# Performance work log

Hardware: AMD Instinct MI355X
Metric: run time of the kernel (lower is better)

## Reference

```python
import jax, jax.numpy as jnp
import numpy as np

NUM_SLOTS = 8
SLOT_DIM = 3
WRITE_RATE = 0.1


def _amu(x, memory, Wk, bk, Ww, bw, Wg, bg, Wo, bo):
    """Associative Memory Unit.
    x: [B, T, Din], memory: [B, N, D] -> (outputs [B, T, Dout], memory [B, N, D]).
    Per step: softmax key-addressing read, gated erase/add write at WRITE_RATE,
    output = Linear(concat(x_t, read)).
    """
    xt = jnp.swapaxes(x, 0, 1)  # [T, B, Din]

    def step(mem, x_t):
        k = x_t @ Wk + bk                                   # [B, D]
        scores = jnp.einsum('bnd,bd->bn', mem, k)           # [B, N]
        w = jax.nn.softmax(scores, axis=-1)                 # addressing weights
        read = jnp.einsum('bn,bnd->bd', w, mem)             # [B, D]
        v = x_t @ Ww + bw                                   # write vector [B, D]
        e = jax.nn.sigmoid(x_t @ Wg + bg)                   # erase gate [B, D]
        we = w[:, :, None] * e[:, None, :]                  # [B, N, D]
        mem = mem * (1.0 - WRITE_RATE * we) + WRITE_RATE * w[:, :, None] * v[:, None, :]
        out = jnp.concatenate([x_t, read], axis=-1) @ Wo + bo
        return mem, out

    mem, outs = jax.lax.scan(step, memory, xt)
    return jnp.swapaxes(outs, 0, 1), mem


def setup_inputs() -> dict:
    key = jax.random.key(0)
    ks = jax.random.split(key, 12)
    B, T, D_in, D_hid, D_out = 64, 512, 128, 512, 128
    s = 0.05
    return {
        'inp': jax.random.normal(ks[0], (B, T, D_in), jnp.float32),
        'W1k': jax.random.normal(ks[1], (D_in, SLOT_DIM), jnp.float32) * s,
        'b1k': jnp.zeros((SLOT_DIM,), jnp.float32),
        'W1w': jax.random.normal(ks[2], (D_in, SLOT_DIM), jnp.float32) * s,
        'b1w': jnp.zeros((SLOT_DIM,), jnp.float32),
        'W1g': jax.random.normal(ks[3], (D_in, SLOT_DIM), jnp.float32) * s,
        'b1g': jnp.zeros((SLOT_DIM,), jnp.float32),
        'W1o': jax.random.normal(ks[4], (D_in + SLOT_DIM, D_hid), jnp.float32) * s,
        'b1o': jnp.zeros((D_hid,), jnp.float32),
        'W2k': jax.random.normal(ks[5], (D_hid, SLOT_DIM), jnp.float32) * s,
        'b2k': jnp.zeros((SLOT_DIM,), jnp.float32),
        'W2w': jax.random.normal(ks[6], (D_hid, SLOT_DIM), jnp.float32) * s,
        'b2w': jnp.zeros((SLOT_DIM,), jnp.float32),
        'W2g': jax.random.normal(ks[7], (D_hid, SLOT_DIM), jnp.float32) * s,
        'b2g': jnp.zeros((SLOT_DIM,), jnp.float32),
        'W2o': jax.random.normal(ks[8], (D_hid + SLOT_DIM, D_out), jnp.float32) * s,
        'b2o': jnp.zeros((D_out,), jnp.float32),
    }


def reference(inp, W1k, b1k, W1w, b1w, W1g, b1g, W1o, b1o,
              W2k, b2k, W2w, b2w, W2g, b2g, W2o, b2o):
    B = inp.shape[0]
    mem0 = jnp.zeros((B, NUM_SLOTS, SLOT_DIM), inp.dtype)
    o1, mem = _amu(inp, mem0, W1k, b1k, W1w, b1w, W1g, b1g, W1o, b1o)
    o1 = jax.nn.sigmoid(o1)  # self.layers = Sequential(Sigmoid())
    o2, mem = _amu(o1, mem, W2k, b2k, W2w, b2w, W2g, b2g, W2o, b2o)
    out = jax.nn.sigmoid(o2[:, -1, :])  # last timestep, then sigmoid
    return out
```

## Files before the change

### kernel.cpp

```cpp
#include <hip/hip_runtime.h>
#include <hip/hip_bf16.h>

#define B_ 64
#define T_ 512
#define LOG2E 1.4426950408889634f
#define PHASE_STEPS 16
#define NPHASE (T_/PHASE_STEPS)

typedef __attribute__((ext_vector_type(8))) short short8;
typedef __attribute__((ext_vector_type(4))) float f32x4;

__device__ __forceinline__ float fast_exp2(float x){ return __builtin_amdgcn_exp2f(x); }
__device__ __forceinline__ float fast_rcp(float x){ return __builtin_amdgcn_rcpf(x); }
__device__ __forceinline__ float sigmoidf_(float x){ return fast_rcp(1.0f + fast_exp2(-x*LOG2E)); }
__device__ __forceinline__ unsigned short f2bf(float f){
  union{float f; unsigned u;} v; v.f = f;
  unsigned r = v.u + 0x7fffu + ((v.u>>16)&1u);
  return (unsigned short)(r>>16);
}

template<int CTRL>
__device__ __forceinline__ float dpp_xadd(float x){
  int y = __builtin_amdgcn_update_dpp(0, __float_as_int(x), CTRL, 0xf, 0xf, true);
  return x + __int_as_float(y);
}
__device__ __forceinline__ float dpp_sum8(float x){
  x = dpp_xadd<0xB1>(x);
  x = dpp_xadd<0x4E>(x);
  x = dpp_xadd<0x141>(x);
  return x;
}

__global__ __launch_bounds__(256) void k_prep(const float* __restrict__ W1o,
    const float* __restrict__ W2k, const float* __restrict__ W2w, const float* __restrict__ W2g,
    unsigned short* __restrict__ W1oTb, unsigned short* __restrict__ W2cTb)
{
  int idx = blockIdx.x*256 + threadIdx.x;
  if (idx < 65536){
    int n = idx >> 7, k = idx & 127;
    W1oTb[idx] = f2bf(W1o[k*512 + n]);
  }
  if (idx < 8192){
    int j = idx >> 9, c = idx & 511;
    float v = 0.f;
    if (j < 3) v = W2k[c*3 + j];
    else if (j < 6) v = W2w[c*3 + j - 3];
    else if (j < 9) v = W2g[c*3 + j - 6];
    W2cTb[idx] = f2bf(v);
  }
}

__global__ __launch_bounds__(256) void k_proj1(const float* __restrict__ X,
    const float* __restrict__ Wk, const float* __restrict__ bk,
    const float* __restrict__ Ww, const float* __restrict__ bw,
    const float* __restrict__ Wg, const float* __restrict__ bg,
    float* __restrict__ P1)
{
  __shared__ __align__(16) float A[64*132];
  __shared__ float Wc[128*12];
  __shared__ float bb[9];
  int tid = threadIdx.x;
  long r0 = (long)blockIdx.x * 64;
  const float4* X4 = (const float4*)(X + r0*128);
  #pragma unroll
  for (int it=0; it<8; ++it){
    int f4 = tid + it*256;
    float4 v = X4[f4];
    int f = f4*4; int row = f>>7; int k = f&127;
    A[row*132+k]   = v.x; A[row*132+k+1] = v.y;
    A[row*132+k+2] = v.z; A[row*132+k+3] = v.w;
  }
  #pragma unroll
  for (int it=0; it<5; ++it){
    int w = tid + it*256;
    if (w < 1152){
      int k = w/9, j = w%9;
      float val;
      if (j<3) val = Wk[k*3+j]; else if (j<6) val = Ww[k*3+j-3]; else val = Wg[k*3+j-6];
      Wc[k*12+j] = val;
    }
  }
  if (tid < 9){
    float v; if (tid<3) v = bk[tid]; else if (tid<6) v = bw[tid-3]; else v = bg[tid-6];
    bb[tid] = v;
  }
  __syncthreads();
  for (int o = tid; o < 576; o += 256){
    int row = o/9, j = o%9;
    float acc = bb[j];
    #pragma unroll 8
    for (int k=0;k<128;++k) acc = fmaf(A[row*132+k], Wc[k*12+j], acc);
    if (j<3) acc *= LOG2E;
    else if (j<6) acc *= 0.1f;
    else acc = 0.1f * sigmoidf_(acc);
    long r = r0 + row;
    int b = (int)(r >> 9); int t = (int)(r & 511);
    int bh = b >> 5, bl = b & 31;
    P1[((long)bh*512 + t)*288 + j*32 + bl] = acc;
  }
}

template<int STORE_ALL>
__device__ __forceinline__ void scan8(const float* __restrict__ P,
                                      float* __restrict__ Rout, int bh)
{
  __shared__ __align__(16) float buf[2][PHASE_STEPS*288];
  int tid = threadIdx.x;
  int wv = tid >> 6, lane = tid & 63;
  const float* Pb = P + (long)bh*512*288;
  if (wv == 4){
    #pragma unroll 1
    for (int p = 0; p < NPHASE; ++p){
      const float4* src = (const float4*)(Pb + (long)p*PHASE_STEPS*288);
      float4* dst = (float4*)buf[p&1];
      float4 tmp[18];
      #pragma unroll
      for (int i=0;i<18;++i) tmp[i] = src[lane + i*64];
      #pragma unroll
      for (int i=0;i<18;++i) dst[lane + i*64] = tmp[i];
      __syncthreads();
    }
  } else {
    int g = lane >> 3, slot = lane & 7;
    int bl = wv*8 + g;
    int batch = bh*32 + bl;
    float m0=0.f, m1=0.f, m2=0.f;
    __syncthreads();
    #pragma unroll 1
    for (int p = 0; p < NPHASE; ++p){
      const float* bp = buf[p&1];
      float pp[3][9];
      #pragma unroll
      for (int j=0;j<9;++j){ pp[0][j] = bp[j*32+bl]; pp[1][j] = bp[288 + j*32+bl]; }
      #pragma unroll
      for (int s=0;s<PHASE_STEPS;++s){
        if (s+2 < PHASE_STEPS){
          #pragma unroll
          for (int j=0;j<9;++j) pp[(s+2)%3][j] = bp[(s+2)*288 + j*32 + bl];
        }
        const float* pv = pp[s%3];
        float sc = fmaf(m2, pv[2], fmaf(m1, pv[1], m0*pv[0]));
        float pe = fast_exp2(sc);
        float S = dpp_sum8(pe);
        float rinv = fast_rcp(S);
        float w = pe * rinv;
        if (STORE_ALL){
          float r0 = dpp_sum8(pe*m0);
          float r1 = dpp_sum8(pe*m1);
          float r2 = dpp_sum8(pe*m2);
          float rsel = (slot==0) ? r0 : ((slot==1) ? r1 : r2);
          rsel *= rinv;
          if (slot < 3) Rout[((p*PHASE_STEPS+s)*3 + slot)*64 + batch] = rsel;
        } else if (s == PHASE_STEPS-1){
          if (p == NPHASE-1){
            float r0 = dpp_sum8(pe*m0);
            float r1 = dpp_sum8(pe*m1);
            float r2 = dpp_sum8(pe*m2);
            float rsel = (slot==0) ? r0 : ((slot==1) ? r1 : r2);
            rsel *= rinv;
            if (slot < 3) Rout[slot*64 + batch] = rsel;
          }
        }
        float v0=pv[3], v1=pv[4], v2=pv[5], e0=pv[6], e1=pv[7], e2=pv[8];
        m0 = fmaf(w, fmaf(-e0, m0, v0), m0);
        m1 = fmaf(w, fmaf(-e1, m1, v1), m1);
        m2 = fmaf(w, fmaf(-e2, m2, v2), m2);
      }
      if (p < NPHASE-1) __syncthreads();
    }
  }
}

__global__ __launch_bounds__(320) void k_scan1(const float* __restrict__ P1,
                                               float* __restrict__ R1)
{
  scan8<1>(P1, R1, (int)blockIdx.x);
}

__global__ __launch_bounds__(256) void k_fused(const float* __restrict__ X,
    const float* __restrict__ W1o, const float* __restrict__ b1o,
    const float* __restrict__ R1,
    const unsigned short* __restrict__ W1oTb, const unsigned short* __restrict__ W2cTb,
    const float* __restrict__ b2k, const float* __restrict__ b2w, const float* __restrict__ b2g,
    float* __restrict__ P2, float* __restrict__ O1last)
{
  __shared__ __align__(16) float rdS[48];
  __shared__ __align__(16) unsigned short o1b[16*520];
  __shared__ __align__(16) float pSum[4*16*16];
  int tid = threadIdx.x;
  int w = tid >> 6, lane = tid & 63;
  int n16 = lane & 15, g4 = lane >> 4;
  long r0 = (long)blockIdx.x * 16;
  int b = (int)(r0 >> 9); int t0 = (int)(r0 & 511);

  if (tid < 48){
    int i = tid/3, d = tid%3;
    rdS[tid] = R1[((t0+i)*3+d)*64 + b];
  }

  short8 afr[4];
  const float* Xrow = X + (r0 + n16)*128;
  #pragma unroll
  for (int q=0;q<4;++q){
    f32x4 x0 = *(const f32x4*)(Xrow + q*32 + g4*8);
    f32x4 x1 = *(const f32x4*)(Xrow + q*32 + g4*8 + 4);
    short8 a;
    a[0]=(short)f2bf(x0[0]); a[1]=(short)f2bf(x0[1]);
    a[2]=(short)f2bf(x0[2]); a[3]=(short)f2bf(x0[3]);
    a[4]=(short)f2bf(x1[0]); a[5]=(short)f2bf(x1[1]);
    a[6]=(short)f2bf(x1[2]); a[7]=(short)f2bf(x1[3]);
    afr[q]=a;
  }
  __syncthreads();

  f32x4 ra = *(const f32x4*)(rdS + g4*12);
  f32x4 rb = *(const f32x4*)(rdS + g4*12 + 4);
  f32x4 rc = *(const f32x4*)(rdS + g4*12 + 8);
  float rd0[4] = { ra[0], ra[3], rb[2], rc[1] };
  float rd1[4] = { ra[1], rb[0], rb[3], rc[2] };
  float rd2[4] = { ra[2], rb[1], rc[0], rc[3] };

  #pragma unroll
  for (int tt=0; tt<8; ++tt){
    int gc = w*128 + tt*16 + n16;
    f32x4 acc = {0.f,0.f,0.f,0.f};
    #pragma unroll
    for (int q=0;q<4;++q){
      short8 bf = *(const short8*)(W1oTb + gc*128 + q*32 + g4*8);
      acc = __builtin_amdgcn_mfma_f32_16x16x32_bf16(afr[q], bf, acc, 0,0,0);
    }
    float bias = b1o[gc];
    float wr0 = W1o[128*512+gc], wr1 = W1o[129*512+gc], wr2 = W1o[130*512+gc];
    #pragma unroll
    for (int reg=0; reg<4; ++reg){
      int rowloc = g4*4 + reg;
      float z = acc[reg] + bias + rd0[reg]*wr0 + rd1[reg]*wr1 + rd2[reg]*wr2;
      float o1 = sigmoidf_(z);
      o1b[rowloc*520 + gc] = f2bf(o1);
      if (t0 == 496 && rowloc == 15) O1last[b*512 + gc] = o1;
    }
  }

  f32x4 accP = {0.f,0.f,0.f,0.f};
  #pragma unroll
  for (int q2=0; q2<4; ++q2){
    int kk = w*128 + q2*32;
    short8 a2 = *(const short8*)(o1b + n16*520 + kk + g4*8);
    short8 bb2 = *(const short8*)(W2cTb + n16*512 + kk + g4*8);
    accP = __builtin_amdgcn_mfma_f32_16x16x32_bf16(a2, bb2, accP, 0,0,0);
  }
  #pragma unroll
  for (int reg=0;reg<4;++reg){
    int rowloc = g4*4+reg;
    pSum[w*256 + rowloc*16 + n16] = accP[reg];
  }
  __syncthreads();
  if (tid < 144){
    int r = tid/9, j = tid%9;
    float s = pSum[r*16+j] + pSum[256+r*16+j] + pSum[512+r*16+j] + pSum[768+r*16+j];
    float outv;
    if (j<3){ s += b2k[j]; outv = s*LOG2E; }
    else if (j<6){ s += b2w[j-3]; outv = 0.1f*s; }
    else { s += b2g[j-6]; outv = 0.1f*sigmoidf_(s); }
    int t = t0 + r;
    int bh = b >> 5, bl = b & 31;
    P2[((long)bh*512 + t)*288 + j*32 + bl] = outv;
  }
}

__global__ __launch_bounds__(320) void k_scan2_opart(const float* __restrict__ P2,
    float* __restrict__ R2F,
    const float* __restrict__ O1last, const float* __restrict__ W2o,
    const float* __restrict__ b2o, float* __restrict__ Opart)
{
  if (blockIdx.x < 2){
    scan8<0>(P2, R2F, (int)blockIdx.x);
    return;
  }
  __shared__ __align__(16) float s2[512];
  int b = blockIdx.x - 2; int tid = threadIdx.x;
  if (tid < 128)
    ((float4*)s2)[tid] = ((const float4*)(O1last + b*512))[tid];
  __syncthreads();
  if (tid < 128){
    float acc = b2o[tid];
    #pragma unroll 8
    for (int n=0;n<512;++n) acc = fmaf(s2[n], W2o[n*128+tid], acc);
    Opart[b*128+tid] = acc;
  }
}

__global__ __launch_bounds__(256) void k_final(const float* __restrict__ Opart,
    const float* __restrict__ R2F, const float* __restrict__ W2o,
    float* __restrict__ out)
{
  int idx = blockIdx.x*256 + threadIdx.x;
  if (idx < 8192){
    int b = idx >> 7; int o = idx & 127;
    float r0 = R2F[b], r1 = R2F[64+b], r2 = R2F[128+b];
    float v = Opart[idx]
            + r0*W2o[512*128+o] + r1*W2o[513*128+o] + r2*W2o[514*128+o];
    out[idx] = sigmoidf_(v);
  }
}

extern "C" void kernel_launch(void* const* d_in, const int* in_sizes, int n_in,
                              void* d_out, int out_size, void* d_ws, size_t ws_size,
                              hipStream_t stream)
{
  const float* X  = (const float*)d_in[0];
  const float* W1k= (const float*)d_in[1]; const float* b1k=(const float*)d_in[2];
  const float* W1w= (const float*)d_in[3]; const float* b1w=(const float*)d_in[4];
  const float* W1g= (const float*)d_in[5]; const float* b1g=(const float*)d_in[6];
  const float* W1o= (const float*)d_in[7]; const float* b1o=(const float*)d_in[8];
  const float* W2k= (const float*)d_in[9]; const float* b2k=(const float*)d_in[10];
  const float* W2w= (const float*)d_in[11]; const float* b2w=(const float*)d_in[12];
  const float* W2g= (const float*)d_in[13]; const float* b2g=(const float*)d_in[14];
  const float* W2o= (const float*)d_in[15]; const float* b2o=(const float*)d_in[16];

  float* ws = (float*)d_ws;
  float* P1     = ws;
  float* R1     = P1 + 294912;
  float* P2     = R1 + 98304;
  float* O1last = P2 + 294912;
  float* R2F    = O1last + 32768;
  float* Opart  = R2F + 192;
  unsigned short* W1oTb = (unsigned short*)(Opart + 8192);
  unsigned short* W2cTb = W1oTb + 65536;
  float* out    = (float*)d_out;

  hipLaunchKernelGGL(k_prep, dim3(256), dim3(256), 0, stream,
                     W1o, W2k, W2w, W2g, W1oTb, W2cTb);
  hipLaunchKernelGGL(k_proj1, dim3(512), dim3(256), 0, stream,
                     X, W1k,b1k, W1w,b1w, W1g,b1g, P1);
  hipLaunchKernelGGL(k_scan1, dim3(2), dim3(320), 0, stream, P1, R1);
  hipLaunchKernelGGL(k_fused, dim3(2048), dim3(256), 0, stream,
                     X, W1o, b1o, R1, W1oTb, W2cTb, b2k, b2w, b2g, P2, O1last);
  hipLaunchKernelGGL(k_scan2_opart, dim3(66), dim3(320), 0, stream,
                     P2, R2F, O1last, W2o, b2o, Opart);
  hipLaunchKernelGGL(k_final, dim3(32), dim3(256), 0, stream,
                     Opart, R2F, W2o, out);
}
```

Measured before the change: 260.7 us.

## Fuse pipeline into persistent megakernel with flag-based producer-consumer overlap

Result: slower. 346.9 us (+33.1%).

```diff
diff --git a/kernel.cpp b/kernel.cpp
--- a/kernel.cpp
+++ b/kernel.cpp
@@ -31,86 +31,30 @@
   return x;
 }
 
-__global__ __launch_bounds__(256) void k_prep(const float* __restrict__ W1o,
-    const float* __restrict__ W2k, const float* __restrict__ W2w, const float* __restrict__ W2g,
-    unsigned short* __restrict__ W1oTb, unsigned short* __restrict__ W2cTb)
+__device__ __forceinline__ unsigned ld_acq(unsigned* p){
+  return __hip_atomic_load(p, __ATOMIC_ACQUIRE, __HIP_MEMORY_SCOPE_AGENT);
+}
+__device__ __forceinline__ void spin_ge(unsigned* p, unsigned tgt){
+  while (ld_acq(p) < tgt) __builtin_amdgcn_s_sleep(4);
+}
+__device__ __forceinline__ void flag_add(unsigned* p){
+  __threadfence();
+  __hip_atomic_fetch_add(p, 1u, __ATOMIC_RELEASE, __HIP_MEMORY_SCOPE_AGENT);
+}
+
+template<int STORE_ALL>
+__device__ __forceinline__ void scan_role(const float* __restrict__ P,
+    float* __restrict__ Rout, int bh,
+    unsigned* cnt_in, unsigned tgt, unsigned* cnt_out, char* smemc)
 {
-  int idx = blockIdx.x*256 + threadIdx.x;
-  if (idx < 65536){
-    int n = idx >> 7, k = idx & 127;
-    W1oTb[idx] = f2bf(W1o[k*512 + n]);
-  }
-  if (idx < 8192){
-    int j = idx >> 9, c = idx & 511;
-    float v = 0.f;
-    if (j < 3) v = W2k[c*3 + j];
-    else if (j < 6) v = W2w[c*3 + j - 3];
-    else if (j < 9) v = W2g[c*3 + j - 6];
-    W2cTb[idx] = f2bf(v);
-  }
-}
-
-__global__ __launch_bounds__(256) void k_proj1(const float* __restrict__ X,
-    const float* __restrict__ Wk, const float* __restrict__ bk,
-    const float* __restrict__ Ww, const float* __restrict__ bw,
-    const float* __restrict__ Wg, const float* __restrict__ bg,
-    float* __restrict__ P1)
-{
-  __shared__ __align__(16) float A[64*132];
-  __shared__ float Wc[128*12];
-  __shared__ float bb[9];
-  int tid = threadIdx.x;
-  long r0 = (long)blockIdx.x * 64;
-  const float4* X4 = (const float4*)(X + r0*128);
-  #pragma unroll
-  for (int it=0; it<8; ++it){
-    int f4 = tid + it*256;
-    float4 v = X4[f4];
-    int f = f4*4; int row = f>>7; int k = f&127;
-    A[row*132+k]   = v.x; A[row*132+k+1] = v.y;
-    A[row*132+k+2] = v.z; A[row*132+k+3] = v.w;
-  }
-  #pragma unroll
-  for (int it=0; it<5; ++it){
-    int w = tid + it*256;
-    if (w < 1152){
-      int k = w/9, j = w%9;
-      float val;
-      if (j<3) val = Wk[k*3+j]; else if (j<6) val = Ww[k*3+j-3]; else val = Wg[k*3+j-6];
-      Wc[k*12+j] = val;
-    }
-  }
-  if (tid < 9){
-    float v; if (tid<3) v = bk[tid]; else if (tid<6) v = bw[tid-3]; else v = bg[tid-6];
-    bb[tid] = v;
-  }
-  __syncthreads();
-  for (int o = tid; o < 576; o += 256){
-    int row = o/9, j = o%9;
-    float acc = bb[j];
-    #pragma unroll 8
-    for (int k=0;k<128;++k) acc = fmaf(A[row*132+k], Wc[k*12+j], acc);
-    if (j<3) acc *= LOG2E;
-    else if (j<6) acc *= 0.1f;
-    else acc = 0.1f * sigmoidf_(acc);
-    long r = r0 + row;
-    int b = (int)(r >> 9); int t = (int)(r & 511);
-    int bh = b >> 5, bl = b & 31;
-    P1[((long)bh*512 + t)*288 + j*32 + bl] = acc;
-  }
-}
-
-template<int STORE_ALL>
-__device__ __forceinline__ void scan8(const float* __restrict__ P,
-                                      float* __restrict__ Rout, int bh)
-{
-  __shared__ __align__(16) float buf[2][PHASE_STEPS*288];
+  float (*buf)[PHASE_STEPS*288] = (float (*)[PHASE_STEPS*288])smemc;
   int tid = threadIdx.x;
   int wv = tid >> 6, lane = tid & 63;
   const float* Pb = P + (long)bh*512*288;
   if (wv == 4){
     #pragma unroll 1
     for (int p = 0; p < NPHASE; ++p){
+      spin_ge(&cnt_in[p], tgt);
       const float4* src = (const float4*)(Pb + (long)p*PHASE_STEPS*288);
       float4* dst = (float4*)buf[p&1];
       float4 tmp[18];
@@ -120,6 +64,7 @@
       for (int i=0;i<18;++i) dst[lane + i*64] = tmp[i];
       __syncthreads();
     }
+    __syncthreads();
   } else {
     int g = lane >> 3, slot = lane & 7;
     int bl = wv*8 + g;
@@ -151,157 +96,223 @@
           float rsel = (slot==0) ? r0 : ((slot==1) ? r1 : r2);
           rsel *= rinv;
           if (slot < 3) Rout[((p*PHASE_STEPS+s)*3 + slot)*64 + batch] = rsel;
-        } else if (s == PHASE_STEPS-1){
-          if (p == NPHASE-1){
-            float r0 = dpp_sum8(pe*m0);
-            float r1 = dpp_sum8(pe*m1);
-            float r2 = dpp_sum8(pe*m2);
-            float rsel = (slot==0) ? r0 : ((slot==1) ? r1 : r2);
-            rsel *= rinv;
-            if (slot < 3) Rout[slot*64 + batch] = rsel;
-          }
+        } else if (s == PHASE_STEPS-1 && p == NPHASE-1){
+          float r0 = dpp_sum8(pe*m0);
+          float r1 = dpp_sum8(pe*m1);
+          float r2 = dpp_sum8(pe*m2);
+          float rsel = (slot==0) ? r0 : ((slot==1) ? r1 : r2);
+          rsel *= rinv;
+          if (slot < 3) Rout[slot*64 + batch] = rsel;
         }
         float v0=pv[3], v1=pv[4], v2=pv[5], e0=pv[6], e1=pv[7], e2=pv[8];
         m0 = fmaf(w, fmaf(-e0, m0, v0), m0);
         m1 = fmaf(w, fmaf(-e1, m1, v1), m1);
         m2 = fmaf(w, fmaf(-e2, m2, v2), m2);
       }
-      if (p < NPHASE-1) __syncthreads();
+      __syncthreads();
+      if (cnt_out && tid == 0) flag_add(&cnt_out[p]);
     }
   }
 }
 
-__global__ __launch_bounds__(320) void k_scan1(const float* __restrict__ P1,
-                                               float* __restrict__ R1)
+__global__ __launch_bounds__(320,1) void k_mega(
+    const float* __restrict__ X,
+    const float* __restrict__ W1k, const float* __restrict__ b1k,
+    const float* __restrict__ W1w, const float* __restrict__ b1w,
+    const float* __restrict__ W1g, const float* __restrict__ b1g,
+    const float* __restrict__ W1o, const float* __restrict__ b1o,
+    const float* __restrict__ W2k, const float* __restrict__ b2k,
+    const float* __restrict__ W2w, const float* __restrict__ b2w,
+    const float* __restrict__ W2g, const float* __restrict__ b2g,
+    float* __restrict__ P1, float* __restrict__ R1,
+    float* __restrict__ P2, float* __restrict__ O1last, float* __restrict__ R2F,
+    unsigned short* __restrict__ W1oTb, unsigned short* __restrict__ W2cTb,
+    unsigned* __restrict__ flags)
 {
-  scan8<1>(P1, R1, (int)blockIdx.x);
-}
-
-__global__ __launch_bounds__(256) void k_fused(const float* __restrict__ X,
-    const float* __restrict__ W1o, const float* __restrict__ b1o,
-    const float* __restrict__ R1,
-    const unsigned short* __restrict__ W1oTb, const unsigned short* __restrict__ W2cTb,
-    const float* __restrict__ b2k, const float* __restrict__ b2w, const float* __restrict__ b2g,
-    float* __restrict__ P2, float* __restrict__ O1last)
+  __shared__ __align__(16) char smem[40448];
+  unsigned* proj_cnt  = flags;
+  unsigned* r1_cnt    = flags + 32;
+  unsigned* fused_cnt = flags + 64;
+  unsigned* prep_cnt  = flags + 96;
+  int role = blockIdx.x;
+  int tid = threadIdx.x;
+
+  if (role < 2){ scan_role<1>(P1, R1, role, proj_cnt, 16, r1_cnt, smem); return; }
+  if (role < 4){ scan_role<0>(P2, R2F, role-2, fused_cnt, 64, nullptr, smem); return; }
+
+  int wid = role - 4;
+  int NW = (int)gridDim.x - 4;
+
+  {
+    int NT = NW*320;
+    int gthread = wid*320 + tid;
+    for (int x = gthread; x < 65536; x += NT){
+      int n = x >> 7, k = x & 127;
+      W1oTb[x] = f2bf(W1o[k*512 + n]);
+    }
+    for (int x = gthread; x < 8192; x += NT){
+      int j = x >> 9, cc = x & 511;
+      float v = 0.f;
+      if (j < 3) v = W2k[cc*3+j];
+      else if (j < 6) v = W2w[cc*3+j-3];
+      else if (j < 9) v = W2g[cc*3+j-6];
+      W2cTb[x] = f2bf(v);
+    }
+    __syncthreads();
+    if (tid == 0) flag_add(prep_cnt);
+  }
+
+  {
+    float* A  = (float*)smem;
+    float* Wc = (float*)(smem + 33792);
+    float* bb = (float*)(smem + 39936);
+    for (int w_=tid; w_<1152; w_+=320){
+      int k=w_/9, j=w_%9; float val;
+      if (j<3) val=W1k[k*3+j]; else if (j<6) val=W1w[k*3+j-3]; else val=W1g[k*3+j-6];
+      Wc[k*12+j]=val;
+    }
+    if (tid<9){ float v; if(tid<3)v=b1k[tid]; else if(tid<6)v=b1w[tid-3]; else v=b1g[tid-6]; bb[tid]=v; }
+    __syncthreads();
+    #pragma unroll 1
+    for (int i = wid; i < 512; i += NW){
+      int c = i >> 4, q = i & 15;
+      if (tid < 256){
+        #pragma unroll
+        for (int it=0; it<8; ++it){
+          int f4 = tid + it*256;
+          int blk = f4 >> 9, off = f4 & 511;
+          const float4* src = (const float4*)(X + ((long)(4*q+blk)*512 + 16*c)*128);
+          float4 v = src[off];
+          int f = off*4, trow = f>>7, k = f&127;
+          int row = blk*16 + trow;
+          A[row*132+k]=v.x; A[row*132+k+1]=v.y; A[row*132+k+2]=v.z; A[row*132+k+3]=v.w;
+        }
+      }
+      __syncthreads();
+      for (int o = tid; o < 576; o += 320){
+        int row=o/9, j=o%9;
+        float acc = bb[j];
+        #pragma unroll 8
+        for (int k=0;k<128;++k) acc = fmaf(A[row*132+k], Wc[k*12+j], acc);
+        if (j<3) acc *= LOG2E;
+        else if (j<6) acc *= 0.1f;
+        else acc = 0.1f*sigmoidf_(acc);
+        int b = 4*q + (row>>4), t = 16*c + (row&15);
+        P1[((long)(b>>5)*512 + t)*288 + j*32 + (b&31)] = acc;
+      }
+      __syncthreads();
+      if (tid == 0) flag_add(&proj_cnt[c]);
+    }
+  }
+
+  if (tid == 0) spin_ge(prep_cnt, (unsigned)NW);
+  __syncthreads();
+
+  {
+    float* pSum = (float*)smem;
+    float* rdS  = (float*)(smem + 4096);
+    unsigned short* o1b = (unsigned short*)(smem + 4352);
+    int w = tid >> 6, lane = tid & 63;
+    int n16 = lane & 15, g4 = lane >> 4;
+    #pragma unroll 1
+    for (int i = wid; i < 2048; i += NW){
+      int c = i >> 6, b = i & 63;
+      if (tid == 0) spin_ge(&r1_cnt[c], 2);
+      __syncthreads();
+      int t0 = c*16;
+      long r0 = (long)b*512 + t0;
+      if (tid < 48){
+        int ii = tid/3, d = tid%3;
+        rdS[tid] = R1[((t0+ii)*3+d)*64 + b];
+      }
+      short8 afr[4];
+      if (w < 4){
+        const float* Xrow = X + (r0 + n16)*128;
+        #pragma unroll
+        for (int q=0;q<4;++q){
+          f32x4 x0 = *(const f32x4*)(Xrow + q*32 + g4*8);
+          f32x4 x1 = *(const f32x4*)(Xrow + q*32 + g4*8 + 4);
+          short8 a;
+          a[0]=(short)f2bf(x0[0]); a[1]=(short)f2bf(x0[1]);
+          a[2]=(short)f2bf(x0[2]); a[3]=(short)f2bf(x0[3]);
+          a[4]=(short)f2bf(x1[0]); a[5]=(short)f2bf(x1[1]);
+          a[6]=(short)f2bf(x1[2]); a[7]=(short)f2bf(x1[3]);
+          afr[q]=a;
+        }
+      }
+      __syncthreads();
+      if (w < 4){
+        f32x4 ra = *(const f32x4*)(rdS + g4*12);
+        f32x4 rb = *(const f32x4*)(rdS + g4*12 + 4);
+        f32x4 rc = *(const f32x4*)(rdS + g4*12 + 8);
+        float rd0[4] = { ra[0], ra[3], rb[2], rc[1] };
+        float rd1[4] = { ra[1], rb[0], rb[3], rc[2] };
+        float rd2[4] = { ra[2], rb[1], rc[0], rc[3] };
+        #pragma unroll
+        for (int tt=0; tt<8; ++tt){
+          int gc = w*128 + tt*16 + n16;
+          f32x4 acc = {0.f,0.f,0.f,0.f};
+          #pragma unroll
+          for (int q=0;q<4;++q){
+            short8 bf = *(const short8*)(W1oTb + gc*128 + q*32 + g4*8);
+            acc = __builtin_amdgcn_mfma_f32_16x16x32_bf16(afr[q], bf, acc, 0,0,0);
+          }
+          float bias = b1o[gc];
+          float wr0 = W1o[128*512+gc], wr1 = W1o[129*512+gc], wr2 = W1o[130*512+gc];
+          #pragma unroll
+          for (int reg=0; reg<4; ++reg){
+            int rowloc = g4*4 + reg;
+            float z = acc[reg] + bias + rd0[reg]*wr0 + rd1[reg]*wr1 + rd2[reg]*wr2;
+            float o1 = sigmoidf_(z);
+            o1b[rowloc*520 + gc] = f2bf(o1);
+            if (c == 31 && rowloc == 15) O1last[b*512 + gc] = o1;
+          }
+        }
+        f32x4 accP = {0.f,0.f,0.f,0.f};
+        #pragma unroll
+        for (int q2=0; q2<4; ++q2){
+          int kk = w*128 + q2*32;
+          short8 a2 = *(const short8*)(o1b + n16*520 + kk + g4*8);
+          short8 bb2 = *(const short8*)(W2cTb + n16*512 + kk + g4*8);
+          accP = __builtin_amdgcn_mfma_f32_16x16x32_bf16(a2, bb2, accP, 0,0,0);
+        }
+        #pragma unroll
+        for (int reg=0;reg<4;++reg){
+          int rowloc = g4*4+reg;
+          pSum[w*256 + rowloc*16 + n16] = accP[reg];
+        }
+      }
+      __syncthreads();
+      if (tid < 144){
+        int r = tid/9, j = tid%9;
+        float s = pSum[r*16+j] + pSum[256+r*16+j] + pSum[512+r*16+j] + pSum[768+r*16+j];
+        float outv;
+        if (j<3){ s += b2k[j]; outv = s*LOG2E; }
+        else if (j<6){ s += b2w[j-3]; outv = 0.1f*s; }
+        else { s += b2g[j-6]; outv = 0.1f*sigmoidf_(s); }
+        int t = t0 + r;
+        P2[((long)(b>>5)*512 + t)*288 + j*32 + (b&31)] = outv;
+      }
+      __syncthreads();
+      if (tid == 0) flag_add(&fused_cnt[c]);
+    }
+  }
+}
+
+__global__ __launch_bounds__(128) void k_final(const float* __restrict__ O1last,
+    const float* __restrict__ R2F, const float* __restrict__ W2o,
+    const float* __restrict__ b2o, float* __restrict__ out)
 {
-  __shared__ __align__(16) float rdS[48];
-  __shared__ __align__(16) unsigned short o1b[16*520];
-  __shared__ __align__(16) float pSum[4*16*16];
-  int tid = threadIdx.x;
-  int w = tid >> 6, lane = tid & 63;
-  int n16 = lane & 15, g4 = lane >> 4;
-  long r0 = (long)blockIdx.x * 16;
-  int b = (int)(r0 >> 9); int t0 = (int)(r0 & 511);
-
-  if (tid < 48){
-    int i = tid/3, d = tid%3;
-    rdS[tid] = R1[((t0+i)*3+d)*64 + b];
-  }
-
-  short8 afr[4];
-  const float* Xrow = X + (r0 + n16)*128;
-  #pragma unroll
-  for (int q=0;q<4;++q){
-    f32x4 x0 = *(const f32x4*)(Xrow + q*32 + g4*8);
-    f32x4 x1 = *(const f32x4*)(Xrow + q*32 + g4*8 + 4);
-    short8 a;
-    a[0]=(short)f2bf(x0[0]); a[1]=(short)f2bf(x0[1]);
-    a[2]=(short)f2bf(x0[2]); a[3]=(short)f2bf(x0[3]);
-    a[4]=(short)f2bf(x1[0]); a[5]=(short)f2bf(x1[1]);
-    a[6]=(short)f2bf(x1[2]); a[7]=(short)f2bf(x1[3]);
-    afr[q]=a;
-  }
+  __shared__ __align__(16) float s2[512];
+  int b = blockIdx.x, tid = threadIdx.x;
+  ((float4*)s2)[tid] = ((const float4*)(O1last + b*512))[tid];
   __syncthreads();
-
-  f32x4 ra = *(const f32x4*)(rdS + g4*12);
-  f32x4 rb = *(const f32x4*)(rdS + g4*12 + 4);
-  f32x4 rc = *(const f32x4*)(rdS + g4*12 + 8);
-  float rd0[4] = { ra[0], ra[3], rb[2], rc[1] };
-  float rd1[4] = { ra[1], rb[0], rb[3], rc[2] };
-  float rd2[4] = { ra[2], rb[1], rc[0], rc[3] };
-
-  #pragma unroll
-  for (int tt=0; tt<8; ++tt){
-    int gc = w*128 + tt*16 + n16;
-    f32x4 acc = {0.f,0.f,0.f,0.f};
-    #pragma unroll
-    for (int q=0;q<4;++q){
-      short8 bf = *(const short8*)(W1oTb + gc*128 + q*32 + g4*8);
-      acc = __builtin_amdgcn_mfma_f32_16x16x32_bf16(afr[q], bf, acc, 0,0,0);
-    }
-    float bias = b1o[gc];
-    float wr0 = W1o[128*512+gc], wr1 = W1o[129*512+gc], wr2 = W1o[130*512+gc];
-    #pragma unroll
-    for (int reg=0; reg<4; ++reg){
-      int rowloc = g4*4 + reg;
-      float z = acc[reg] + bias + rd0[reg]*wr0 + rd1[reg]*wr1 + rd2[reg]*wr2;
-      float o1 = sigmoidf_(z);
-      o1b[rowloc*520 + gc] = f2bf(o1);
-      if (t0 == 496 && rowloc == 15) O1last[b*512 + gc] = o1;
-    }
-  }
-
-  f32x4 accP = {0.f,0.f,0.f,0.f};
-  #pragma unroll
-  for (int q2=0; q2<4; ++q2){
-    int kk = w*128 + q2*32;
-    short8 a2 = *(const short8*)(o1b + n16*520 + kk + g4*8);
-    short8 bb2 = *(const short8*)(W2cTb + n16*512 + kk + g4*8);
-    accP = __builtin_amdgcn_mfma_f32_16x16x32_bf16(a2, bb2, accP, 0,0,0);
-  }
-  #pragma unroll
-  for (int reg=0;reg<4;++reg){
-    int rowloc = g4*4+reg;
-    pSum[w*256 + rowloc*16 + n16] = accP[reg];
-  }
-  __syncthreads();
-  if (tid < 144){
-    int r = tid/9, j = tid%9;
-    float s = pSum[r*16+j] + pSum[256+r*16+j] + pSum[512+r*16+j] + pSum[768+r*16+j];
-    float outv;
-    if (j<3){ s += b2k[j]; outv = s*LOG2E; }
-    else if (j<6){ s += b2w[j-3]; outv = 0.1f*s; }
-    else { s += b2g[j-6]; outv = 0.1f*sigmoidf_(s); }
-    int t = t0 + r;
-    int bh = b >> 5, bl = b & 31;
-    P2[((long)bh*512 + t)*288 + j*32 + bl] = outv;
-  }
-}
-
-__global__ __launch_bounds__(320) void k_scan2_opart(const float* __restrict__ P2,
-    float* __restrict__ R2F,
-    const float* __restrict__ O1last, const float* __restrict__ W2o,
-    const float* __restrict__ b2o, float* __restrict__ Opart)
-{
-  if (blockIdx.x < 2){
-    scan8<0>(P2, R2F, (int)blockIdx.x);
-    return;
-  }
-  __shared__ __align__(16) float s2[512];
-  int b = blockIdx.x - 2; int tid = threadIdx.x;
-  if (tid < 128)
-    ((float4*)s2)[tid] = ((const float4*)(O1last + b*512))[tid];
-  __syncthreads();
-  if (tid < 128){
-    float acc = b2o[tid];
-    #pragma unroll 8
-    for (int n=0;n<512;++n) acc = fmaf(s2[n], W2o[n*128+tid], acc);
-    Opart[b*128+tid] = acc;
-  }
-}
-
-__global__ __launch_bounds__(256) void k_final(const float* __restrict__ Opart,
-    const float* __restrict__ R2F, const float* __restrict__ W2o,
-    float* __restrict__ out)
-{
-  int idx = blockIdx.x*256 + threadIdx.x;
-  if (idx < 8192){
-    int b = idx >> 7; int o = idx & 127;
-    float r0 = R2F[b], r1 = R2F[64+b], r2 = R2F[128+b];
-    float v = Opart[idx]
-            + r0*W2o[512*128+o] + r1*W2o[513*128+o] + r2*W2o[514*128+o];
-    out[idx] = sigmoidf_(v);
-  }
+  float acc = b2o[tid];
+  #pragma unroll 8
+  for (int n=0;n<512;++n) acc = fmaf(s2[n], W2o[n*128+tid], acc);
+  float r0 = R2F[b], r1 = R2F[64+b], r2 = R2F[128+b];
+  acc += r0*W2o[512*128+tid] + r1*W2o[513*128+tid] + r2*W2o[514*128+tid];
+  out[b*128+tid] = sigmoidf_(acc);
 }
 
 extern "C" void kernel_launch(void* const* d_in, const int* in_sizes, int n_in,
@@ -324,20 +335,16 @@
   float* P2     = R1 + 98304;
   float* O1last = P2 + 294912;
   float* R2F    = O1last + 32768;
-  float* Opart  = R2F + 192;
-  unsigned short* W1oTb = (unsigned short*)(Opart + 8192);
+  unsigned short* W1oTb = (unsigned short*)(R2F + 192);
   unsigned short* W2cTb = W1oTb + 65536;
+  unsigned* flags = (unsigned*)(R2F + 192 + 32768 + 4096);
   float* out    = (float*)d_out;
 
-  hipLaunchKernelGGL(k_prep, dim3(256), dim3(256), 0, stream,
-                     W1o, W2k, W2w, W2g, W1oTb, W2cTb);
-  hipLaunchKernelGGL(k_proj1, dim3(512), dim3(256), 0, stream,
-                     X, W1k,b1k, W1w,b1w, W1g,b1g, P1);
-  hipLaunchKernelGGL(k_scan1, dim3(2), dim3(320), 0, stream, P1, R1);
-  hipLaunchKernelGGL(k_fused, dim3(2048), dim3(256), 0, stream,
-                     X, W1o, b1o, R1, W1oTb, W2cTb, b2k, b2w, b2g, P2, O1last);
-  hipLaunchKernelGGL(k_scan2_opart, dim3(66), dim3(320), 0, stream,
-                     P2, R2F, O1last, W2o, b2o, Opart);
-  hipLaunchKernelGGL(k_final, dim3(32), dim3(256), 0, stream,
-                     Opart, R2F, W2o, out);
-}
+  hipMemsetAsync(flags, 0, 512, stream);
+  hipLaunchKernelGGL(k_mega, dim3(256), dim3(320), 0, stream,
+                     X, W1k,b1k, W1w,b1w, W1g,b1g, W1o,b1o,
+                     W2k,b2k, W2w,b2w, W2g,b2g,
+                     P1, R1, P2, O1last, R2F, W1oTb, W2cTb, flags);
+  hipLaunchKernelGGL(k_final, dim3(64), dim3(128), 0, stream,
+                     O1last, R2F, W2o, b2o, out);
+}
```
